# Optimization experiments

Hardware: AMD Instinct MI355X
Metric: run time of the kernel (lower is better)

## Reference

```python
import jax, jax.numpy as jnp
import numpy as np

B, S, D, H, HZ = 4096, 64, 9, 128, 32
DT = 0.1


def _lstm_cell(x, h, c, Wih, Whh, bih, bhh):
    gates = x @ Wih.T + bih + h @ Whh.T + bhh
    i, f, g, o = jnp.split(gates, 4, axis=-1)
    c_new = jax.nn.sigmoid(f) * c + jax.nn.sigmoid(i) * jnp.tanh(g)
    h_new = jax.nn.sigmoid(o) * jnp.tanh(c_new)
    return h_new, c_new


def _forward(input_batch, W_ih_enc, W_hh_enc, b_ih_enc, b_hh_enc, W_e, V_e, v_e,
             W_d, V_d, v_d, W_ih_dec, W_hh_dec, b_ih_dec, b_hh_dec,
             W_out, b_out, scaler_mean, scaler_std, pos_mean):
    bsz = input_batch.shape[0]
    # ---- encoder with input attention ----
    x_perm = jnp.swapaxes(input_batch, 1, 2)          # (B, D, S)
    attn_input = jnp.einsum('bds,ts->bdt', x_perm, V_e)  # V_e * x^i, precomputed once
    h0 = jnp.zeros((bsz, H), input_batch.dtype)
    c0 = jnp.zeros((bsz, H), input_batch.dtype)

    def enc_step(carry, x_t):
        h, c = carry
        attn_hidden = jnp.concatenate([h, c], axis=1) @ W_e.T          # (B, S)
        comb = jnp.tanh(attn_hidden[:, None, :] + attn_input)          # (B, D, S)
        e = comb @ v_e                                                 # (B, D)
        alpha = jax.nn.softmax(e, axis=1)
        h, c = _lstm_cell(alpha * x_t, h, c, W_ih_enc, W_hh_enc, b_ih_enc, b_hh_enc)
        return (h, c), h

    (h_enc, c_enc), hs = jax.lax.scan(enc_step, (h0, c0), jnp.swapaxes(input_batch, 0, 1))
    enc_hidden = jnp.swapaxes(hs, 0, 1)               # (B, S, H)
    attn_encoder = enc_hidden @ V_d.T                 # V_d * h_j, precomputed once

    # ---- initial physics state ----
    pos = input_batch[:, -1, :3] + pos_mean
    vel = input_batch[:, -1, 3:6] * scaler_std + scaler_mean
    pre_vel = input_batch[:, -2, 3:6] * scaler_std + scaler_mean
    acc = (vel - pre_vel) / DT

    def dec_step(carry, _):
        d, c, pos, vel, acc = carry
        attn_dec = jnp.concatenate([d, c], axis=1) @ W_d.T             # (B, H)
        comb = jnp.tanh(attn_dec[:, None, :] + attn_encoder)           # (B, S, H)
        beta = jax.nn.softmax(comb @ v_d, axis=1)                      # (B, S)
        context = jnp.einsum('bs,bsh->bh', beta, enc_hidden)           # (B, H)
        phys = jnp.concatenate([pos - pos_mean,
                                (vel - scaler_mean) / scaler_std,
                                acc / scaler_std], axis=1)             # (B, 9)
        d, c = _lstm_cell(jnp.concatenate([phys, context], axis=1), d, c,
                          W_ih_dec, W_hh_dec, b_ih_dec, b_hh_dec)
        pred_acc = (jnp.concatenate([d, context], axis=1) @ W_out.T + b_out) * scaler_std
        pos_pred = pos + vel * DT + 0.5 * acc * DT * DT                # Verlet position
        vel_new = vel + 0.5 * (acc + pred_acc) * DT                    # Verlet velocity
        out = jnp.concatenate([pos_pred, vel_new, pred_acc], axis=1)   # (B, 9)
        return (d, c, pos_pred, vel_new, pred_acc), out

    _, outs = jax.lax.scan(dec_step, (h_enc, c_enc, pos, vel, acc), None, length=HZ)
    return jnp.swapaxes(outs, 0, 1)                   # (B, HZ, 9)


def setup_inputs() -> dict:
    key = jax.random.key(0)
    ks = jax.random.split(key, 16)
    p = lambda k, shape, s=0.05: jax.random.normal(k, shape, dtype=jnp.float32) * s
    return dict(
        input_batch=jax.random.normal(ks[0], (B, S, D), dtype=jnp.float32),
        W_ih_enc=p(ks[1], (4 * H, D)), W_hh_enc=p(ks[2], (4 * H, H)),
        b_ih_enc=jnp.zeros((4 * H,), jnp.float32), b_hh_enc=jnp.zeros((4 * H,), jnp.float32),
        W_e=p(ks[3], (S, 2 * H)), V_e=p(ks[4], (S, S)), v_e=p(ks[5], (S,)),
        W_d=p(ks[6], (H, 2 * H)), V_d=p(ks[7], (H, H)), v_d=p(ks[8], (H,)),
        W_ih_dec=p(ks[9], (4 * H, 9 + H)), W_hh_dec=p(ks[10], (4 * H, H)),
        b_ih_dec=jnp.zeros((4 * H,), jnp.float32), b_hh_dec=jnp.zeros((4 * H,), jnp.float32),
        W_out=p(ks[11], (3, 2 * H)), b_out=jnp.zeros((3,), jnp.float32),
        scaler_mean=p(ks[12], (3,), 0.1),
        scaler_std=jnp.abs(p(ks[13], (3,), 0.1)) + 1.0,
        pos_mean=p(ks[14], (3,), 0.1),
    )


def reference(input_batch, W_ih_enc, W_hh_enc, b_ih_enc, b_hh_enc, W_e, V_e, v_e,
              W_d, V_d, v_d, W_ih_dec, W_hh_dec, b_ih_dec, b_hh_dec,
              W_out, b_out, scaler_mean, scaler_std, pos_mean):
    return _forward(input_batch, W_ih_enc, W_hh_enc, b_ih_enc, b_hh_enc, W_e, V_e, v_e,
                    W_d, V_d, v_d, W_ih_dec, W_hh_dec, b_ih_dec, b_hh_dec,
                    W_out, b_out, scaler_mean, scaler_std, pos_mean)
```

## Files before the change

### kernel.cpp

```cpp
#include <hip/hip_runtime.h>
#include <hip/hip_bf16.h>
#include <hip/hip_fp8.h>

#define B_   4096
#define S_   64
#define D_   9
#define H_   128
#define HZ_  32
#define DT_  0.1f

#define OFF_WET    0
#define OFF_VET    16384
#define OFF_WENCT  20480
#define OFF_BENC   90624
#define OFF_WDT    91136
#define OFF_WDECT  123904
#define OFF_BDEC   259584
#define OFF_WOUTT  260096
#define OFF_VDT    260864
#define OFF_DECD   277248
#define OFF_DECC   801536
#define F32_TOTAL  1325824
#define PREP_N     277248


typedef __bf16 bf16x8 __attribute__((ext_vector_type(8)));
typedef float  f32x4  __attribute__((ext_vector_type(4)));

__device__ __forceinline__ float fast_tanh(float x) {
    float e = __expf(2.0f * x);
    return 1.0f - __fdividef(2.0f, e + 1.0f);
}
__device__ __forceinline__ float sigf(float x) {
    return __fdividef(1.0f, 1.0f + __expf(-x));
}
__device__ __forceinline__ float bf_lo(unsigned int u) { return __uint_as_float(u << 16); }
__device__ __forceinline__ float bf_hi(unsigned int u) { return __uint_as_float(u & 0xffff0000u); }
__device__ __forceinline__ float bfu2f(unsigned short u) { return __uint_as_float((unsigned int)u << 16); }
__device__ __forceinline__ unsigned short f2bfu(float f) {
    __hip_bfloat16 b = __float2bfloat16(f);
    return *(unsigned short*)&b;
}
__device__ __forceinline__ unsigned int pack_bf(float lo, float hi) {
    return (unsigned int)f2bfu(lo) | ((unsigned int)f2bfu(hi) << 16);
}
__device__ __forceinline__ float f8tof(unsigned int byte) {
    __hip_fp8_e4m3 t; t.__x = (unsigned char)byte; return (float)t;
}
__device__ __forceinline__ unsigned char f2f8(float f) {
    __hip_fp8_e4m3 q(f); return q.__x;
}
__device__ __forceinline__ unsigned int pack4_f8(float a, float b, float c, float d) {
    return (unsigned int)f2f8(a) | ((unsigned int)f2f8(b) << 8) |
           ((unsigned int)f2f8(c) << 16) | ((unsigned int)f2f8(d) << 24);
}

__global__ void prep_kernel(const float* __restrict__ Wih_e, const float* __restrict__ Whh_e,
    const float* __restrict__ bih_e, const float* __restrict__ bhh_e,
    const float* __restrict__ W_e, const float* __restrict__ V_e,
    const float* __restrict__ W_d, const float* __restrict__ V_d,
    const float* __restrict__ Wih_d, const float* __restrict__ Whh_d,
    const float* __restrict__ bih_d, const float* __restrict__ bhh_d,
    const float* __restrict__ W_out, float* __restrict__ ws) {
  for (int idx = blockIdx.x * blockDim.x + threadIdx.x; idx < PREP_N;
       idx += gridDim.x * blockDim.x) {
    int i = idx;
    if (i < 16384) { continue; }
    i -= 16384;
    if (i < 4096) { int s = i >> 6, t = i & 63; ws[OFF_VET + i] = V_e[t * 64 + s]; continue; }
    i -= 4096;
    if (i < 70144) { continue; }
    i -= 70144;
    if (i < 512) { ws[OFF_BENC + i] = bih_e[i] + bhh_e[i]; continue; }
    i -= 512;
    if (i < 32768) { continue; }
    i -= 32768;
    if (i < 135680) { continue; }
    i -= 135680;
    if (i < 512) { ws[OFF_BDEC + i] = bih_d[i] + bhh_d[i]; continue; }
    i -= 512;
    if (i < 768) { int k = i / 3, j = i % 3; ws[OFF_WOUTT + i] = W_out[j * 256 + k]; continue; }
  }
}

__global__ void prep_mfma_kernel(const float* __restrict__ W_d,
    const float* __restrict__ Wih_d, const float* __restrict__ Whh_d,
    unsigned short* __restrict__ WdTm, unsigned short* __restrict__ WdecTm) {
  int idx = blockIdx.x * blockDim.x + threadIdx.x;
  if (idx < 32768) {
    int j = idx & 7, l = (idx >> 3) & 63, t = idx >> 9;
    int nt = t & 7, ks = t >> 3;
    int k = ks * 32 + (l >> 4) * 8 + j;
    int n = nt * 16 + (l & 15);
    WdTm[idx] = f2bfu(W_d[n * 256 + k]);
    return;
  }
  int i2 = idx - 32768;
  if (i2 < 147456) {
    int j = i2 & 7, l = (i2 >> 3) & 63, t = i2 >> 9;
    int ks = t % 9, tile = t / 9;
    int q = tile & 3, is = tile >> 2;
    int k = ks * 32 + (l >> 4) * 8 + j;
    int g = q * 128 + is * 16 + (l & 15);
    float v;
    if (k < 128)      v = Whh_d[g * 128 + k];
    else if (k < 256) v = Wih_d[g * 137 + 9 + (k - 128)];
    else if (k < 265) v = Wih_d[g * 137 + (k - 256)];
    else              v = 0.f;
    WdecTm[i2] = f2bfu(v);
  }
}

__global__ void prep_enc_mfma_kernel(const float* __restrict__ W_e,
    const float* __restrict__ Wih_e, const float* __restrict__ Whh_e,
    const float* __restrict__ V_d,
    unsigned short* __restrict__ WeTm, unsigned short* __restrict__ WencTm,
    unsigned short* __restrict__ VdTm) {
  int idx = blockIdx.x * blockDim.x + threadIdx.x;
  if (idx < 16384) {
    int j = idx & 7, l = (idx >> 3) & 63, tile = idx >> 9;
    int nt = tile & 3, ks = tile >> 2;
    int k = ks * 32 + (l >> 4) * 8 + j;
    int n = nt * 16 + (l & 15);
    WeTm[idx] = f2bfu(W_e[n * 256 + k]);
    return;
  }
  int i2 = idx - 16384;
  if (i2 < 81920) {
    int j = i2 & 7, l = (i2 >> 3) & 63, tile = i2 >> 9;
    int ks = tile % 5, tq = tile / 5;
    int q = tq & 3, is = tq >> 2;
    int kk = (l >> 4) * 8 + j;
    int g = q * 128 + is * 16 + (l & 15);
    float v;
    if (ks < 4) v = Whh_e[g * 128 + ks * 32 + kk];
    else        v = (kk < 9) ? Wih_e[g * 9 + kk] : 0.f;
    WencTm[i2] = f2bfu(v);
    return;
  }
  int i3 = i2 - 81920;
  if (i3 < 16384) {
    int j = i3 & 7, l = (i3 >> 3) & 63, tile = i3 >> 9;
    int nt = tile & 7, ks = tile >> 3;
    int i = ks * 32 + (l >> 4) * 8 + j;
    int n = nt * 16 + (l & 15);
    VdTm[i3] = f2bfu(V_d[n * 128 + i]);
  }
}

__global__ __launch_bounds__(512, 1) void encoder_mfma_kernel(
    const float* __restrict__ x_in, const float* __restrict__ ws,
    const float* __restrict__ v_e_g,
    const unsigned short* __restrict__ WeTm, const unsigned short* __restrict__ WencTm,
    __hip_bfloat16* __restrict__ EH,
    unsigned short* __restrict__ dG, float* __restrict__ cG) {
  __shared__ unsigned short hA[2][16 * 296];
  __shared__ float cF[16 * 132];
  __shared__ float ahL[16 * 64];
  __shared__ unsigned short aiL[16 * 576];
  __shared__ unsigned short xbL[16 * 576];

  const int tid = threadIdx.x;
  const int b0 = blockIdx.x * 16;
  const int l = tid & 63, w = tid >> 6;
  const int quad = l >> 4, l15 = l & 15;

  for (int i = tid; i < 16 * 576; i += 512) {
    int m = i / 576, r = i % 576;
    xbL[i] = f2bfu(x_in[(size_t)(b0 + m) * 576 + r]);
  }
  for (int i = tid; i < 2 * 16 * 296; i += 512) ((unsigned short*)hA)[i] = 0;
  for (int i = tid; i < 16 * 132; i += 512) cF[i] = 0.f;
  __syncthreads();

  {
    const float* __restrict__ VeT = ws + OFF_VET;
    for (int i = tid; i < 16 * 576; i += 512) {
      int t = i & 63, dd = (i >> 6) % 9, m = i / 576;
      float acc = 0.f;
      for (int s = 0; s < 64; ++s) acc += bfu2f(xbL[m * 576 + s * 9 + dd]) * VeT[s * 64 + t];
      aiL[m * 576 + dd * 64 + t] = f2bfu(acc);
    }
  }
  const float ve_r = v_e_g[l];
  const int ig = w * 16 + l15;
  float bbq[4];
  #pragma unroll
  for (int q = 0; q < 4; ++q) bbq[q] = ws[OFF_BENC + q * 128 + ig];
  __syncthreads();

  for (int t = 0; t < S_; ++t) {
    unsigned short* bufC = hA[t & 1];
    unsigned short* bufN = hA[(t + 1) & 1];
    if (w < 4) {
      f32x4 acc = {0.f, 0.f, 0.f, 0.f};
      #pragma unroll
      for (int ks = 0; ks < 8; ++ks) {
        uint4 au = *(const uint4*)&bufC[l15 * 296 + ks * 32 + quad * 8];
        uint4 bu = *(const uint4*)(WeTm + (size_t)((ks * 4 + w) * 64 + l) * 8);
        acc = __builtin_amdgcn_mfma_f32_16x16x32_bf16(
            __builtin_bit_cast(bf16x8, au), __builtin_bit_cast(bf16x8, bu), acc, 0, 0, 0);
      }
      #pragma unroll
      for (int r = 0; r < 4; ++r)
        ahL[(quad * 4 + r) * 64 + w * 16 + l15] = acc[r];
    }
    __syncthreads();
    {
      const int m0 = 2 * w, m1 = 2 * w + 1;
      float a0 = ahL[m0 * 64 + l], a1 = ahL[m1 * 64 + l];
      float e0k = -1e30f, e1k = -1e30f;
      #pragma unroll
      for (int dd = 0; dd < 9; ++dd) {
        float t0 = fast_tanh(a0 + bfu2f(aiL[m0 * 576 + dd * 64 + l])) * ve_r;
        float t1 = fast_tanh(a1 + bfu2f(aiL[m1 * 576 + dd * 64 + l])) * ve_r;
        #pragma unroll
        for (int off = 32; off; off >>= 1) {
          t0 += __shfl_xor(t0, off, 64);
          t1 += __shfl_xor(t1, off, 64);
        }
        if (l == dd) { e0k = t0; e1k = t1; }
      }
      float mx0 = e0k, mx1 = e1k;
      #pragma unroll
      for (int off = 8; off; off >>= 1) {
        mx0 = fmaxf(mx0, __shfl_xor(mx0, off, 64));
        mx1 = fmaxf(mx1, __shfl_xor(mx1, off, 64));
      }
      float ex0 = (l < 9) ? __expf(e0k - mx0) : 0.f;
      float ex1 = (l < 9) ? __expf(e1k - mx1) : 0.f;
      float s0 = ex0, s1 = ex1;
      #pragma unroll
      for (int off = 8; off; off >>= 1) {
        s0 += __shfl_xor(s0, off, 64);
        s1 += __shfl_xor(s1, off, 64);
      }
      if (l < 9) {
        bufC[m0 * 296 + 256 + l] = f2bfu(__fdividef(ex0, s0) * bfu2f(xbL[m0 * 576 + t * 9 + l]));
        bufC[m1 * 296 + 256 + l] = f2bfu(__fdividef(ex1, s1) * bfu2f(xbL[m1 * 576 + t * 9 + l]));
      }
    }
    __syncthreads();
    {
      uint4 af[5];
      #pragma unroll
      for (int ks = 0; ks < 4; ++ks)
        af[ks] = *(const uint4*)&bufC[l15 * 296 + ks * 32 + quad * 8];
      af[4] = *(const uint4*)&bufC[l15 * 296 + 256 + quad * 8];
      f32x4 g4[4];
      #pragma unroll
      for (int q = 0; q < 4; ++q) {
        f32x4 acc = {0.f, 0.f, 0.f, 0.f};
        #pragma unroll
        for (int ks = 0; ks < 5; ++ks) {
          uint4 bu = *(const uint4*)(WencTm + (size_t)(((w * 4 + q) * 5 + ks) * 64 + l) * 8);
          acc = __builtin_amdgcn_mfma_f32_16x16x32_bf16(
              __builtin_bit_cast(bf16x8, af[ks]), __builtin_bit_cast(bf16x8, bu), acc, 0, 0, 0);
        }
        g4[q] = acc;
      }
      #pragma unroll
      for (int r = 0; r < 4; ++r) {
        int m = quad * 4 + r;
        float gi = g4[0][r] + bbq[0];
        float gf = g4[1][r] + bbq[1];
        float gg = g4[2][r] + bbq[2];
        float go = g4[3][r] + bbq[3];
        float co = cF[m * 132 + ig];
        float cn = sigf(gf) * co + sigf(gi) * fast_tanh(gg);
        float hn = sigf(go) * fast_tanh(cn);
        cF[m * 132 + ig] = cn;
        bufN[m * 296 + ig] = f2bfu(hn);
        bufN[m * 296 + 128 + ig] = f2bfu(cn);
        EH[((size_t)(b0 + m) * S_ + t) * H_ + ig] = __float2bfloat16(hn);
      }
    }
    __syncthreads();
  }
  for (int i = tid; i < 16 * 128; i += 512) {
    int m = i >> 7, ii = i & 127;
    dG[(size_t)(b0 + m) * 128 + ii] = hA[0][m * 296 + ii];
    cG[(size_t)(b0 + m) * 128 + ii] = cF[m * 132 + ii];
  }
}

__global__ __launch_bounds__(256) void attnenc_mfma_kernel(
    const unsigned short* __restrict__ EH, const unsigned short* __restrict__ VdTm,
    unsigned char* __restrict__ AETf8, unsigned char* __restrict__ EHf8) {
  const int tid = threadIdx.x;
  const int b = blockIdx.x * 4 + (tid >> 6);
  const int l = tid & 63;
  const int quad = l >> 4, l15 = l & 15;

  const unsigned short* ehb = EH + (size_t)b * 8192;
  uint4 A[4][4];
  #pragma unroll
  for (int st = 0; st < 4; ++st)
    #pragma unroll
    for (int ks = 0; ks < 4; ++ks)
      A[st][ks] = *(const uint4*)(ehb + (st * 16 + l15) * 128 + ks * 32 + quad * 8);

  {
    unsigned char* e8b = EHf8 + (size_t)b * 8192;
    #pragma unroll
    for (int st = 0; st < 4; ++st)
      #pragma unroll
      for (int ks = 0; ks < 4; ++ks) {
        uint4 a = A[st][ks];
        uint2 pk;
        pk.x = pack4_f8(bf_lo(a.x), bf_hi(a.x), bf_lo(a.y), bf_hi(a.y));
        pk.y = pack4_f8(bf_lo(a.z), bf_hi(a.z), bf_lo(a.w), bf_hi(a.w));
        *(uint2*)(e8b + (st * 16 + l15) * 128 + ks * 32 + quad * 8) = pk;
      }
  }

  unsigned char* outb = AETf8 + (size_t)b * 8192;
  const int k = l15;
  #pragma unroll
  for (int nt = 0; nt < 8; ++nt) {
    uint4 Bf[4];
    #pragma unroll
    for (int ks = 0; ks < 4; ++ks)
      Bf[ks] = *(const uint4*)(VdTm + (size_t)((ks * 8 + nt) * 64 + l) * 8);
    int kg = nt * 16 + k;
    int kb = kg >> 3, k7 = kg & 7;
    #pragma unroll
    for (int st = 0; st < 4; ++st) {
      f32x4 acc = {0.f, 0.f, 0.f, 0.f};
      #pragma unroll
      for (int ks = 0; ks < 4; ++ks)
        acc = __builtin_amdgcn_mfma_f32_16x16x32_bf16(
            __builtin_bit_cast(bf16x8, A[st][ks]), __builtin_bit_cast(bf16x8, Bf[ks]), acc, 0, 0, 0);
      #pragma unroll
      for (int r = 0; r < 4; ++r) {
        int s = st * 16 + quad * 4 + r;
        outb[kb * 512 + s * 8 + k7] = f2f8(acc[r]);
      }
    }
  }
}

__global__ __launch_bounds__(256) void init_dec_kernel(
    const float* __restrict__ x_in,
    const unsigned short* __restrict__ dG, const float* __restrict__ cG,
    const unsigned short* __restrict__ WdTm,
    const float* __restrict__ smean_g, const float* __restrict__ sstd_g,
    const float* __restrict__ pmean_g,
    unsigned short* __restrict__ adG, float* __restrict__ pvsG) {
  __shared__ unsigned short dcB[16 * 264];
  const int tid = threadIdx.x;
  const int b0 = blockIdx.x * 16;
  const int l = tid & 63, w = tid >> 6;
  const int quad = l >> 4, l15 = l & 15;

  {
    int m = tid >> 4, i0 = (tid & 15) * 8;
    *(uint4*)&dcB[m * 264 + i0] = *(const uint4*)(dG + (size_t)(b0 + m) * 128 + i0);
    float4 c0 = *(const float4*)(cG + (size_t)(b0 + m) * 128 + i0);
    float4 c1 = *(const float4*)(cG + (size_t)(b0 + m) * 128 + i0 + 4);
    uint4 pk;
    pk.x = pack_bf(c0.x, c0.y); pk.y = pack_bf(c0.z, c0.w);
    pk.z = pack_bf(c1.x, c1.y); pk.w = pack_bf(c1.z, c1.w);
    *(uint4*)&dcB[m * 264 + 128 + i0] = pk;
  }
  if (tid < 48) {
    int m = tid / 3, jj = tid % 3;
    const float* xi = x_in + (size_t)(b0 + m) * 576;
    float sm = smean_g[jj], ss = sstd_g[jj], pm = pmean_g[jj];
    float v  = xi[63 * 9 + 3 + jj] * ss + sm;
    float pv = xi[62 * 9 + 3 + jj] * ss + sm;
    float* P = pvsG + (size_t)(b0 + m) * 12;
    P[jj] = xi[63 * 9 + jj] + pm;
    P[3 + jj] = v;
    P[6 + jj] = (v - pv) / DT_;
  }
  __syncthreads();
  #pragma unroll
  for (int t = 0; t < 2; ++t) {
    const int nt = w + 4 * t;
    f32x4 acc = {0.f, 0.f, 0.f, 0.f};
    #pragma unroll
    for (int ks = 0; ks < 8; ++ks) {
      uint4 au = *(const uint4*)&dcB[l15 * 264 + ks * 32 + quad * 8];
      uint4 bu = *(const uint4*)(WdTm + (size_t)((ks * 8 + nt) * 64 + l) * 8);
      acc = __builtin_amdgcn_mfma_f32_16x16x32_bf16(
          __builtin_bit_cast(bf16x8, au), __builtin_bit_cast(bf16x8, bu), acc, 0, 0, 0);
    }
    int n = nt * 16 + l15;
    #pragma unroll
    for (int r = 0; r < 4; ++r)
      adG[(size_t)(b0 + quad * 4 + r) * 128 + n] = f2bfu(acc[r]);
  }
}

__global__ __launch_bounds__(256, 8) void attn_step_kernel(
    const unsigned char* __restrict__ AETf8, const unsigned char* __restrict__ EHf8,
    const unsigned short* __restrict__ adG, const float* __restrict__ v_d_g,
    unsigned short* __restrict__ ctxG) {
  __shared__ unsigned short adL[2 * 128];
  __shared__ float vdL[128];
  __shared__ float scp[2][2][64];
  __shared__ float bet[2][64];
  __shared__ float ctxP[2][2][128];

  const int tid = threadIdx.x;
  const int b0 = blockIdx.x * 2;
  const int l = tid & 63, w = tid >> 6;
  const int ml = w >> 1, half = w & 1;
  const int quad = l >> 4, l15 = l & 15;

  if (tid < 32)
    *(uint4*)&adL[tid * 8] = *(const uint4*)(adG + (size_t)(b0 + (tid >> 4)) * 128 + (tid & 15) * 8);
  if (tid < 128) vdL[tid] = v_d_g[tid];
  __syncthreads();

  {
    const unsigned char* aet = AETf8 + (size_t)(b0 + ml) * 8192 + (size_t)half * 8 * 512;
    const unsigned short* adp = adL + ml * 128 + half * 64;
    float e = 0.f;
    #pragma unroll
    for (int kb = 0; kb < 8; ++kb) {
      uint2 av = *(const uint2*)(aet + kb * 512 + l * 8);
      uint4 ad8 = *(const uint4*)(adp + kb * 8);
      float4 v0 = *(const float4*)&vdL[half * 64 + kb * 8];
      float4 v1 = *(const float4*)&vdL[half * 64 + kb * 8 + 4];
      e += fast_tanh(bf_lo(ad8.x) + f8tof(av.x))       * v0.x;
      e += fast_tanh(bf_hi(ad8.x) + f8tof(av.x >> 8))  * v0.y;
      e += fast_tanh(bf_lo(ad8.y) + f8tof(av.x >> 16)) * v0.z;
      e += fast_tanh(bf_hi(ad8.y) + f8tof(av.x >> 24)) * v0.w;
      e += fast_tanh(bf_lo(ad8.z) + f8tof(av.y))       * v1.x;
      e += fast_tanh(bf_hi(ad8.z) + f8tof(av.y >> 8))  * v1.y;
      e += fast_tanh(bf_lo(ad8.w) + f8tof(av.y >> 16)) * v1.z;
      e += fast_tanh(bf_hi(ad8.w) + f8tof(av.y >> 24)) * v1.w;
    }
    scp[ml][half][l] = e;
  }
  __syncthreads();
  if (half == 0) {
    float e = scp[ml][0][l] + scp[ml][1][l];
    float mx = e;
    #pragma unroll
    for (int off = 32; off; off >>= 1) mx = fmaxf(mx, __shfl_xor(mx, off, 64));
    float ex = __expf(e - mx);
    float ss = ex;
    #pragma unroll
    for (int off = 32; off; off >>= 1) ss += __shfl_xor(ss, off, 64);
    bet[ml][l] = __fdividef(ex, ss);
  }
  __syncthreads();
  {
    const unsigned char* base = EHf8 + (size_t)(b0 + ml) * 8192 + (size_t)half * 32 * 128;
    float a[8];
    #pragma unroll
    for (int r = 0; r < 8; ++r) a[r] = 0.f;
    #pragma unroll
    for (int it = 0; it < 8; ++it) {
      int sl = it * 4 + quad;
      uint2 ev = *(const uint2*)(base + sl * 128 + l15 * 8);
      float bt = bet[ml][half * 32 + sl];
      a[0] += bt * f8tof(ev.x);       a[1] += bt * f8tof(ev.x >> 8);
      a[2] += bt * f8tof(ev.x >> 16); a[3] += bt * f8tof(ev.x >> 24);
      a[4] += bt * f8tof(ev.y);       a[5] += bt * f8tof(ev.y >> 8);
      a[6] += bt * f8tof(ev.y >> 16); a[7] += bt * f8tof(ev.y >> 24);
    }
    #pragma unroll
    for (int r = 0; r < 8; ++r) {
      a[r] += __shfl_xor(a[r], 16, 64);
      a[r] += __shfl_xor(a[r], 32, 64);
    }
    if (quad == 0) {
      *(float4*)&ctxP[ml][half][l15 * 8]     = make_float4(a[0], a[1], a[2], a[3]);
      *(float4*)&ctxP[ml][half][l15 * 8 + 4] = make_float4(a[4], a[5], a[6], a[7]);
    }
  }
  __syncthreads();
  if (tid < 128) {
    int mi = tid >> 6, hp = (tid & 63) * 2;
    float c0 = ctxP[mi][0][hp]     + ctxP[mi][1][hp];
    float c1 = ctxP[mi][0][hp + 1] + ctxP[mi][1][hp + 1];
    *(unsigned int*)(ctxG + (size_t)(b0 + mi) * 128 + hp) = pack_bf(c0, c1);
  }
}

__global__ __launch_bounds__(512, 2) void gemm_step_kernel(
    const float* __restrict__ ws,
    const unsigned short* __restrict__ dG_in, float* __restrict__ cG,
    const unsigned short* __restrict__ ctxG,
    const unsigned short* __restrict__ WdTm, const unsigned short* __restrict__ WdecTm,
    unsigned short* __restrict__ dG_out, unsigned short* __restrict__ adG,
    float* __restrict__ pvsG,
    const float* __restrict__ b_out_g, const float* __restrict__ smean_g,
    const float* __restrict__ sstd_g, const float* __restrict__ pmean_g,
    float* __restrict__ out, int hz) {
  __shared__ unsigned short gA[16 * 296];
  __shared__ unsigned short dcB[16 * 264];
  __shared__ float pd[16 * 3 * 8];
  __shared__ float pc[16 * 3 * 4];

  const int tid = threadIdx.x;
  const int b0 = blockIdx.x * 16;
  const int l = tid & 63, w = tid >> 6;
  const int quad = l >> 4, l15 = l & 15;

  if (tid < 256) {
    int m = tid >> 4, i0 = (tid & 15) * 8;
    *(uint4*)&gA[m * 296 + i0] = *(const uint4*)(dG_in + (size_t)(b0 + m) * 128 + i0);
  } else {
    int t = tid - 256;
    int m = t >> 4, i0 = (t & 15) * 8;
    *(uint4*)&gA[m * 296 + 128 + i0] = *(const uint4*)(ctxG + (size_t)(b0 + m) * 128 + i0);
  }
  if (tid < 496) { int mm = tid / 31, r = tid % 31; gA[mm * 296 + 265 + r] = 0; }
  if (tid < 48) {
    int m = tid / 3, jj = tid % 3;
    const float* P = pvsG + (size_t)(b0 + m) * 12;
    float sm = smean_g[jj], ss = sstd_g[jj], pm = pmean_g[jj];
    gA[m * 296 + 256 + jj]     = f2bfu(P[jj] - pm);
    gA[m * 296 + 256 + 3 + jj] = f2bfu((P[3 + jj] - sm) / ss);
    gA[m * 296 + 256 + 6 + jj] = f2bfu(P[6 + jj] / ss);
  }
  __syncthreads();

  {
    uint4 af[9];
    #pragma unroll
    for (int ks = 0; ks < 9; ++ks)
      af[ks] = *(const uint4*)&gA[l15 * 296 + ks * 32 + quad * 8];
    const int is = w, i = is * 16 + l15;
    float bb[4], wd[3];
    #pragma unroll
    for (int q = 0; q < 4; ++q) bb[q] = ws[OFF_BDEC + q * 128 + i];
    #pragma unroll
    for (int jj = 0; jj < 3; ++jj) wd[jj] = ws[OFF_WOUTT + i * 3 + jj];
    f32x4 g4[4];
    #pragma unroll
    for (int q = 0; q < 4; ++q) {
      f32x4 acc = {0.f, 0.f, 0.f, 0.f};
      #pragma unroll
      for (int ks = 0; ks < 9; ++ks) {
        uint4 bu = *(const uint4*)(WdecTm + (size_t)(((is * 4 + q) * 9 + ks) * 64 + l) * 8);
        acc = __builtin_amdgcn_mfma_f32_16x16x32_bf16(
            __builtin_bit_cast(bf16x8, af[ks]), __builtin_bit_cast(bf16x8, bu), acc, 0, 0, 0);
      }
      g4[q] = acc;
    }
    float pr[4][3];
    #pragma unroll
    for (int r = 0; r < 4; ++r) {
      int m = quad * 4 + r;
      float gi = g4[0][r] + bb[0];
      float gf = g4[1][r] + bb[1];
      float gg = g4[2][r] + bb[2];
      float go = g4[3][r] + bb[3];
      float co = cG[(size_t)(b0 + m) * 128 + i];
      float cn = sigf(gf) * co + sigf(gi) * fast_tanh(gg);
      float hn = sigf(go) * fast_tanh(cn);
      cG[(size_t)(b0 + m) * 128 + i] = cn;
      unsigned short hb = f2bfu(hn);
      dG_out[(size_t)(b0 + m) * 128 + i] = hb;
      dcB[m * 264 + i] = hb;
      dcB[m * 264 + 128 + i] = f2bfu(cn);
      pr[r][0] = hn * wd[0]; pr[r][1] = hn * wd[1]; pr[r][2] = hn * wd[2];
    }
    #pragma unroll
    for (int r = 0; r < 4; ++r)
      #pragma unroll
      for (int jj = 0; jj < 3; ++jj) {
        float v = pr[r][jj];
        #pragma unroll
        for (int off = 8; off; off >>= 1) v += __shfl_xor(v, off, 64);
        pr[r][jj] = v;
      }
    if (l15 == 0) {
      #pragma unroll
      for (int r = 0; r < 4; ++r)
        #pragma unroll
        for (int jj = 0; jj < 3; ++jj)
          pd[((quad * 4 + r) * 3 + jj) * 8 + is] = pr[r][jj];
    }
  }
  __syncthreads();

  {
    const int nt = w;
    f32x4 acc = {0.f, 0.f, 0.f, 0.f};
    #pragma unroll
    for (int ks = 0; ks < 8; ++ks) {
      uint4 au = *(const uint4*)&dcB[l15 * 264 + ks * 32 + quad * 8];
      uint4 bu = *(const uint4*)(WdTm + (size_t)((ks * 8 + nt) * 64 + l) * 8);
      acc = __builtin_amdgcn_mfma_f32_16x16x32_bf16(
          __builtin_bit_cast(bf16x8, au), __builtin_bit_cast(bf16x8, bu), acc, 0, 0, 0);
    }
    int n = nt * 16 + l15;
    #pragma unroll
    for (int r = 0; r < 4; ++r) {
      int m = quad * 4 + r;
      adG[(size_t)(b0 + m) * 128 + n] = f2bfu(acc[r]);
    }
  }
  if (tid < 192) {
    int m = tid / 12, jj = (tid % 12) / 4, part = tid % 4;
    int k0 = part * 32;
    float acc = 0.f;
    for (int k = k0; k < k0 + 32; ++k) {
      __hip_bfloat16 hv = *(__hip_bfloat16*)&gA[m * 296 + 128 + k];
      acc += __bfloat162float(hv) * ws[OFF_WOUTT + 384 + k * 3 + jj];
    }
    pc[(m * 3 + jj) * 4 + part] = acc;
  }
  __syncthreads();

  if (tid < 48) {
    int m = tid / 3, jj = tid % 3;
    float s = b_out_g[jj];
    #pragma unroll
    for (int p = 0; p < 4; ++p) s += pc[(m * 3 + jj) * 4 + p];
    #pragma unroll
    for (int is = 0; is < 8; ++is) s += pd[(m * 3 + jj) * 8 + is];
    float pacc = s * sstd_g[jj];
    float* P = pvsG + (size_t)(b0 + m) * 12;
    float pos = P[jj], vel = P[3 + jj], acc = P[6 + jj];
    float ppred = pos + vel * DT_ + 0.5f * acc * DT_ * DT_;
    float vnew  = vel + 0.5f * (acc + pacc) * DT_;
    size_t ob = ((size_t)(b0 + m) * HZ_ + hz) * 9;
    out[ob + jj] = ppred; out[ob + 3 + jj] = vnew; out[ob + 6 + jj] = pacc;
    P[jj] = ppred; P[3 + jj] = vnew; P[6 + jj] = pacc;
  }
}

extern "C" void kernel_launch(void* const* d_in, const int* in_sizes, int n_in,
                              void* d_out, int out_size, void* d_ws, size_t ws_size,
                              hipStream_t stream) {
  (void)in_sizes; (void)n_in; (void)out_size; (void)ws_size;
  const float* x      = (const float*)d_in[0];
  const float* Wih_e  = (const float*)d_in[1];
  const float* Whh_e  = (const float*)d_in[2];
  const float* bih_e  = (const float*)d_in[3];
  const float* bhh_e  = (const float*)d_in[4];
  const float* W_e    = (const float*)d_in[5];
  const float* V_e    = (const float*)d_in[6];
  const float* v_e    = (const float*)d_in[7];
  const float* W_d    = (const float*)d_in[8];
  const float* V_d    = (const float*)d_in[9];
  const float* v_d    = (const float*)d_in[10];
  const float* Wih_d  = (const float*)d_in[11];
  const float* Whh_d  = (const float*)d_in[12];
  const float* bih_d  = (const float*)d_in[13];
  const float* bhh_d  = (const float*)d_in[14];
  const float* W_out  = (const float*)d_in[15];
  const float* b_out  = (const float*)d_in[16];
  const float* smean  = (const float*)d_in[17];
  const float* sstd   = (const float*)d_in[18];
  const float* pmean  = (const float*)d_in[19];

  float* ws = (float*)d_ws;
  float* pvsG = ws;
  unsigned short* WeTm   = (unsigned short*)(ws + OFF_WET);
  unsigned short* WencTm = (unsigned short*)(ws + OFF_WENCT);
  unsigned short* WdTm   = (unsigned short*)(ws + OFF_WDT);
  unsigned short* WdecTm = (unsigned short*)(ws + OFF_WDECT);
  unsigned short* VdTm   = (unsigned short*)(ws + OFF_VDT);
  unsigned short* dG     = (unsigned short*)(ws + OFF_DECD);
  unsigned short* ctxG   = dG + 524288;
  float* cG = ws + OFF_DECC;
  unsigned short* ub  = (unsigned short*)(ws + F32_TOTAL);
  unsigned short* EH  = ub;
  unsigned char*  AETf8 = (unsigned char*)(ub + 33554432);
  unsigned char*  EHf8  = AETf8 + (size_t)B_ * 8192;
  unsigned short* adG = ub + 67108864;
  float* out = (float*)d_out;

  prep_kernel<<<(PREP_N + 255) / 256, 256, 0, stream>>>(
      Wih_e, Whh_e, bih_e, bhh_e, W_e, V_e, W_d, V_d,
      Wih_d, Whh_d, bih_d, bhh_d, W_out, ws);
  prep_mfma_kernel<<<(32768 + 147456 + 255) / 256, 256, 0, stream>>>(
      W_d, Wih_d, Whh_d, WdTm, WdecTm);
  prep_enc_mfma_kernel<<<(16384 + 81920 + 16384 + 255) / 256, 256, 0, stream>>>(
      W_e, Wih_e, Whh_e, V_d, WeTm, WencTm, VdTm);
  encoder_mfma_kernel<<<B_ / 16, 512, 0, stream>>>(
      x, ws, v_e, WeTm, WencTm, (__hip_bfloat16*)EH, dG, cG);
  attnenc_mfma_kernel<<<B_ / 4, 256, 0, stream>>>(EH, VdTm, AETf8, EHf8);
  init_dec_kernel<<<B_ / 16, 256, 0, stream>>>(
      x, dG, cG, WdTm, smean, sstd, pmean, adG, pvsG);
  for (int hz = 0; hz < HZ_; ++hz) {
    attn_step_kernel<<<B_ / 2, 256, 0, stream>>>(AETf8, EHf8, adG, v_d, ctxG);
    gemm_step_kernel<<<B_ / 16, 512, 0, stream>>>(
        ws, dG, cG, ctxG, WdTm, WdecTm, dG, adG, pvsG,
        b_out, smean, sstd, pmean, out, hz);
  }
}
```

Measured before the change: 1.687 ms.

## Fuse decoder init and all horizon steps into one persistent kernel

Replaces the per-step attention and GEMM kernel launches (64 launches plus init) with a single kernel in which each block owns 4 batch rows and loops over all 32 horizon steps. The attention-encoder tile and the decoder hidden, cell and physics state stay in shared memory instead of round-tripping through global memory between launches. The cost is MFMA tiles that are only a quarter full (4 of 16 rows used), so weight loads per row rise, and the large shared-memory footprint limits occupancy to few blocks per CU.

```diff
diff --git a/kernel.cpp b/kernel.cpp
--- a/kernel.cpp
+++ b/kernel.cpp
@@ -22,7 +22,6 @@
 #define OFF_DECC   801536
 #define F32_TOTAL  1325824
 #define PREP_N     277248
-
 
 typedef __bf16 bf16x8 __attribute__((ext_vector_type(8)));
 typedef float  f32x4  __attribute__((ext_vector_type(4)));
@@ -340,44 +339,86 @@
   }
 }
 
-__global__ __launch_bounds__(256) void init_dec_kernel(
-    const float* __restrict__ x_in,
+__global__ __launch_bounds__(256, 2) void dec_fused_kernel(
+    const float* __restrict__ ws,
+    const unsigned char* __restrict__ AETf8, const unsigned char* __restrict__ EHf8,
     const unsigned short* __restrict__ dG, const float* __restrict__ cG,
-    const unsigned short* __restrict__ WdTm,
+    const unsigned short* __restrict__ WdTm, const unsigned short* __restrict__ WdecTm,
+    const float* __restrict__ v_d_g, const float* __restrict__ b_out_g,
     const float* __restrict__ smean_g, const float* __restrict__ sstd_g,
     const float* __restrict__ pmean_g,
-    unsigned short* __restrict__ adG, float* __restrict__ pvsG) {
+    const float* __restrict__ x_in,
+    float* __restrict__ out) {
+  __shared__ unsigned char  AET[4][8192];
+  __shared__ unsigned short gA[16 * 296];
   __shared__ unsigned short dcB[16 * 264];
+  __shared__ float          cL[4 * 128];
+  __shared__ unsigned short adL[4 * 128];
+  __shared__ float          bet[4][64];
+  __shared__ float          vdL[128];
+  __shared__ float          pcs[4 * 3 * 8];
+  __shared__ float          pvs[4 * 12];
+
   const int tid = threadIdx.x;
-  const int b0 = blockIdx.x * 16;
+  const int b0 = blockIdx.x * 4;
   const int l = tid & 63, w = tid >> 6;
   const int quad = l >> 4, l15 = l & 15;
 
+  for (int i = tid; i < 16 * 296; i += 256) gA[i] = 0;
+  for (int i = tid; i < 16 * 264; i += 256) dcB[i] = 0;
   {
+    const uint4* src = (const uint4*)(AETf8 + (size_t)b0 * 8192);
+    uint4* dst = (uint4*)AET;
+    for (int i = tid; i < 2048; i += 256) dst[i] = src[i];
+  }
+  if (tid < 128) vdL[tid] = v_d_g[tid];
+  __syncthreads();
+
+  if (tid < 64) {
     int m = tid >> 4, i0 = (tid & 15) * 8;
-    *(uint4*)&dcB[m * 264 + i0] = *(const uint4*)(dG + (size_t)(b0 + m) * 128 + i0);
+    uint4 dv = *(const uint4*)(dG + (size_t)(b0 + m) * 128 + i0);
+    *(uint4*)&gA[m * 296 + i0] = dv;
+    *(uint4*)&dcB[m * 264 + i0] = dv;
     float4 c0 = *(const float4*)(cG + (size_t)(b0 + m) * 128 + i0);
     float4 c1 = *(const float4*)(cG + (size_t)(b0 + m) * 128 + i0 + 4);
+    *(float4*)&cL[m * 128 + i0] = c0;
+    *(float4*)&cL[m * 128 + i0 + 4] = c1;
     uint4 pk;
     pk.x = pack_bf(c0.x, c0.y); pk.y = pack_bf(c0.z, c0.w);
     pk.z = pack_bf(c1.x, c1.y); pk.w = pack_bf(c1.z, c1.w);
     *(uint4*)&dcB[m * 264 + 128 + i0] = pk;
   }
-  if (tid < 48) {
+  if (tid < 12) {
     int m = tid / 3, jj = tid % 3;
     const float* xi = x_in + (size_t)(b0 + m) * 576;
     float sm = smean_g[jj], ss = sstd_g[jj], pm = pmean_g[jj];
     float v  = xi[63 * 9 + 3 + jj] * ss + sm;
     float pv = xi[62 * 9 + 3 + jj] * ss + sm;
-    float* P = pvsG + (size_t)(b0 + m) * 12;
-    P[jj] = xi[63 * 9 + jj] + pm;
-    P[3 + jj] = v;
-    P[6 + jj] = (v - pv) / DT_;
+    float pos = xi[63 * 9 + jj] + pm;
+    float ac = (v - pv) / DT_;
+    float* P = pvs + m * 12;
+    P[jj] = pos; P[3 + jj] = v; P[6 + jj] = ac;
+    gA[m * 296 + 256 + jj]     = f2bfu(pos - pm);
+    gA[m * 296 + 256 + 3 + jj] = f2bfu((v - sm) / ss);
+    gA[m * 296 + 256 + 6 + jj] = f2bfu(ac / ss);
+  }
+  float bb[2][4];
+  #pragma unroll
+  for (int t2 = 0; t2 < 2; ++t2) {
+    int i = (w + 4 * t2) * 16 + l15;
+    #pragma unroll
+    for (int q = 0; q < 4; ++q) bb[t2][q] = ws[OFF_BDEC + q * 128 + i];
+  }
+  float k_sm = 0.f, k_ss = 1.f, k_pm = 0.f, k_bo = 0.f;
+  if (tid < 12) {
+    int jj = tid % 3;
+    k_sm = smean_g[jj]; k_ss = sstd_g[jj]; k_pm = pmean_g[jj]; k_bo = b_out_g[jj];
   }
   __syncthreads();
+
   #pragma unroll
-  for (int t = 0; t < 2; ++t) {
-    const int nt = w + 4 * t;
+  for (int t2 = 0; t2 < 2; ++t2) {
+    const int nt = w + 4 * t2;
     f32x4 acc = {0.f, 0.f, 0.f, 0.f};
     #pragma unroll
     for (int ks = 0; ks < 8; ++ks) {
@@ -386,245 +427,161 @@
       acc = __builtin_amdgcn_mfma_f32_16x16x32_bf16(
           __builtin_bit_cast(bf16x8, au), __builtin_bit_cast(bf16x8, bu), acc, 0, 0, 0);
     }
-    int n = nt * 16 + l15;
-    #pragma unroll
-    for (int r = 0; r < 4; ++r)
-      adG[(size_t)(b0 + quad * 4 + r) * 128 + n] = f2bfu(acc[r]);
-  }
-}
-
-__global__ __launch_bounds__(256, 8) void attn_step_kernel(
-    const unsigned char* __restrict__ AETf8, const unsigned char* __restrict__ EHf8,
-    const unsigned short* __restrict__ adG, const float* __restrict__ v_d_g,
-    unsigned short* __restrict__ ctxG) {
-  __shared__ unsigned short adL[2 * 128];
-  __shared__ float vdL[128];
-  __shared__ float scp[2][2][64];
-  __shared__ float bet[2][64];
-  __shared__ float ctxP[2][2][128];
-
-  const int tid = threadIdx.x;
-  const int b0 = blockIdx.x * 2;
-  const int l = tid & 63, w = tid >> 6;
-  const int ml = w >> 1, half = w & 1;
-  const int quad = l >> 4, l15 = l & 15;
-
-  if (tid < 32)
-    *(uint4*)&adL[tid * 8] = *(const uint4*)(adG + (size_t)(b0 + (tid >> 4)) * 128 + (tid & 15) * 8);
-  if (tid < 128) vdL[tid] = v_d_g[tid];
+    if (quad == 0) {
+      int n = nt * 16 + l15;
+      #pragma unroll
+      for (int r = 0; r < 4; ++r) adL[r * 128 + n] = f2bfu(acc[r]);
+    }
+  }
   __syncthreads();
 
-  {
-    const unsigned char* aet = AETf8 + (size_t)(b0 + ml) * 8192 + (size_t)half * 8 * 512;
-    const unsigned short* adp = adL + ml * 128 + half * 64;
-    float e = 0.f;
-    #pragma unroll
-    for (int kb = 0; kb < 8; ++kb) {
-      uint2 av = *(const uint2*)(aet + kb * 512 + l * 8);
-      uint4 ad8 = *(const uint4*)(adp + kb * 8);
-      float4 v0 = *(const float4*)&vdL[half * 64 + kb * 8];
-      float4 v1 = *(const float4*)&vdL[half * 64 + kb * 8 + 4];
-      e += fast_tanh(bf_lo(ad8.x) + f8tof(av.x))       * v0.x;
-      e += fast_tanh(bf_hi(ad8.x) + f8tof(av.x >> 8))  * v0.y;
-      e += fast_tanh(bf_lo(ad8.y) + f8tof(av.x >> 16)) * v0.z;
-      e += fast_tanh(bf_hi(ad8.y) + f8tof(av.x >> 24)) * v0.w;
-      e += fast_tanh(bf_lo(ad8.z) + f8tof(av.y))       * v1.x;
-      e += fast_tanh(bf_hi(ad8.z) + f8tof(av.y >> 8))  * v1.y;
-      e += fast_tanh(bf_lo(ad8.w) + f8tof(av.y >> 16)) * v1.z;
-      e += fast_tanh(bf_hi(ad8.w) + f8tof(av.y >> 24)) * v1.w;
-    }
-    scp[ml][half][l] = e;
-  }
-  __syncthreads();
-  if (half == 0) {
-    float e = scp[ml][0][l] + scp[ml][1][l];
-    float mx = e;
-    #pragma unroll
-    for (int off = 32; off; off >>= 1) mx = fmaxf(mx, __shfl_xor(mx, off, 64));
-    float ex = __expf(e - mx);
-    float ss = ex;
-    #pragma unroll
-    for (int off = 32; off; off >>= 1) ss += __shfl_xor(ss, off, 64);
-    bet[ml][l] = __fdividef(ex, ss);
-  }
-  __syncthreads();
-  {
-    const unsigned char* base = EHf8 + (size_t)(b0 + ml) * 8192 + (size_t)half * 32 * 128;
-    float a[8];
-    #pragma unroll
-    for (int r = 0; r < 8; ++r) a[r] = 0.f;
-    #pragma unroll
-    for (int it = 0; it < 8; ++it) {
-      int sl = it * 4 + quad;
-      uint2 ev = *(const uint2*)(base + sl * 128 + l15 * 8);
-      float bt = bet[ml][half * 32 + sl];
-      a[0] += bt * f8tof(ev.x);       a[1] += bt * f8tof(ev.x >> 8);
-      a[2] += bt * f8tof(ev.x >> 16); a[3] += bt * f8tof(ev.x >> 24);
-      a[4] += bt * f8tof(ev.y);       a[5] += bt * f8tof(ev.y >> 8);
-      a[6] += bt * f8tof(ev.y >> 16); a[7] += bt * f8tof(ev.y >> 24);
-    }
-    #pragma unroll
-    for (int r = 0; r < 8; ++r) {
-      a[r] += __shfl_xor(a[r], 16, 64);
-      a[r] += __shfl_xor(a[r], 32, 64);
-    }
-    if (quad == 0) {
-      *(float4*)&ctxP[ml][half][l15 * 8]     = make_float4(a[0], a[1], a[2], a[3]);
-      *(float4*)&ctxP[ml][half][l15 * 8 + 4] = make_float4(a[4], a[5], a[6], a[7]);
-    }
-  }
-  __syncthreads();
-  if (tid < 128) {
-    int mi = tid >> 6, hp = (tid & 63) * 2;
-    float c0 = ctxP[mi][0][hp]     + ctxP[mi][1][hp];
-    float c1 = ctxP[mi][0][hp + 1] + ctxP[mi][1][hp + 1];
-    *(unsigned int*)(ctxG + (size_t)(b0 + mi) * 128 + hp) = pack_bf(c0, c1);
-  }
-}
-
-__global__ __launch_bounds__(512, 2) void gemm_step_kernel(
-    const float* __restrict__ ws,
-    const unsigned short* __restrict__ dG_in, float* __restrict__ cG,
-    const unsigned short* __restrict__ ctxG,
-    const unsigned short* __restrict__ WdTm, const unsigned short* __restrict__ WdecTm,
-    unsigned short* __restrict__ dG_out, unsigned short* __restrict__ adG,
-    float* __restrict__ pvsG,
-    const float* __restrict__ b_out_g, const float* __restrict__ smean_g,
-    const float* __restrict__ sstd_g, const float* __restrict__ pmean_g,
-    float* __restrict__ out, int hz) {
-  __shared__ unsigned short gA[16 * 296];
-  __shared__ unsigned short dcB[16 * 264];
-  __shared__ float pd[16 * 3 * 8];
-  __shared__ float pc[16 * 3 * 4];
-
-  const int tid = threadIdx.x;
-  const int b0 = blockIdx.x * 16;
-  const int l = tid & 63, w = tid >> 6;
-  const int quad = l >> 4, l15 = l & 15;
-
-  if (tid < 256) {
-    int m = tid >> 4, i0 = (tid & 15) * 8;
-    *(uint4*)&gA[m * 296 + i0] = *(const uint4*)(dG_in + (size_t)(b0 + m) * 128 + i0);
-  } else {
-    int t = tid - 256;
-    int m = t >> 4, i0 = (t & 15) * 8;
-    *(uint4*)&gA[m * 296 + 128 + i0] = *(const uint4*)(ctxG + (size_t)(b0 + m) * 128 + i0);
-  }
-  if (tid < 496) { int mm = tid / 31, r = tid % 31; gA[mm * 296 + 265 + r] = 0; }
-  if (tid < 48) {
-    int m = tid / 3, jj = tid % 3;
-    const float* P = pvsG + (size_t)(b0 + m) * 12;
-    float sm = smean_g[jj], ss = sstd_g[jj], pm = pmean_g[jj];
-    gA[m * 296 + 256 + jj]     = f2bfu(P[jj] - pm);
-    gA[m * 296 + 256 + 3 + jj] = f2bfu((P[3 + jj] - sm) / ss);
-    gA[m * 296 + 256 + 6 + jj] = f2bfu(P[6 + jj] / ss);
-  }
-  __syncthreads();
-
-  {
+  for (int hz = 0; hz < HZ_; ++hz) {
+    {
+      const unsigned char* aet = AET[w];
+      float e = 0.f;
+      #pragma unroll
+      for (int kb = 0; kb < 16; ++kb) {
+        uint2 av = *(const uint2*)(aet + kb * 512 + l * 8);
+        uint4 ad8 = *(const uint4*)(adL + w * 128 + kb * 8);
+        float4 v0 = *(const float4*)&vdL[kb * 8];
+        float4 v1 = *(const float4*)&vdL[kb * 8 + 4];
+        e += fast_tanh(bf_lo(ad8.x) + f8tof(av.x))       * v0.x;
+        e += fast_tanh(bf_hi(ad8.x) + f8tof(av.x >> 8))  * v0.y;
+        e += fast_tanh(bf_lo(ad8.y) + f8tof(av.x >> 16)) * v0.z;
+        e += fast_tanh(bf_hi(ad8.y) + f8tof(av.x >> 24)) * v0.w;
+        e += fast_tanh(bf_lo(ad8.z) + f8tof(av.y))       * v1.x;
+        e += fast_tanh(bf_hi(ad8.z) + f8tof(av.y >> 8))  * v1.y;
+        e += fast_tanh(bf_lo(ad8.w) + f8tof(av.y >> 16)) * v1.z;
+        e += fast_tanh(bf_hi(ad8.w) + f8tof(av.y >> 24)) * v1.w;
+      }
+      float mx = e;
+      #pragma unroll
+      for (int off = 32; off; off >>= 1) mx = fmaxf(mx, __shfl_xor(mx, off, 64));
+      float ex = __expf(e - mx);
+      float sm = ex;
+      #pragma unroll
+      for (int off = 32; off; off >>= 1) sm += __shfl_xor(sm, off, 64);
+      bet[w][l] = __fdividef(ex, sm);
+    }
+    __syncthreads();
+
+    {
+      const unsigned char* ehb = EHf8 + (size_t)(b0 + w) * 8192;
+      const int i0 = l15 * 8;
+      float a[8];
+      #pragma unroll
+      for (int r = 0; r < 8; ++r) a[r] = 0.f;
+      #pragma unroll
+      for (int it = 0; it < 16; ++it) {
+        int s = quad * 16 + it;
+        uint2 ev = *(const uint2*)(ehb + s * 128 + i0);
+        float bt = bet[w][s];
+        a[0] += bt * f8tof(ev.x);       a[1] += bt * f8tof(ev.x >> 8);
+        a[2] += bt * f8tof(ev.x >> 16); a[3] += bt * f8tof(ev.x >> 24);
+        a[4] += bt * f8tof(ev.y);       a[5] += bt * f8tof(ev.y >> 8);
+        a[6] += bt * f8tof(ev.y >> 16); a[7] += bt * f8tof(ev.y >> 24);
+      }
+      #pragma unroll
+      for (int r = 0; r < 8; ++r) {
+        a[r] += __shfl_xor(a[r], 16, 64);
+        a[r] += __shfl_xor(a[r], 32, 64);
+      }
+      if (quad == 0) {
+        uint4 pk;
+        pk.x = pack_bf(a[0], a[1]); pk.y = pack_bf(a[2], a[3]);
+        pk.z = pack_bf(a[4], a[5]); pk.w = pack_bf(a[6], a[7]);
+        *(uint4*)&gA[w * 296 + 128 + i0] = pk;
+      }
+    }
+    __syncthreads();
+
     uint4 af[9];
     #pragma unroll
     for (int ks = 0; ks < 9; ++ks)
       af[ks] = *(const uint4*)&gA[l15 * 296 + ks * 32 + quad * 8];
-    const int is = w, i = is * 16 + l15;
-    float bb[4], wd[3];
-    #pragma unroll
-    for (int q = 0; q < 4; ++q) bb[q] = ws[OFF_BDEC + q * 128 + i];
-    #pragma unroll
-    for (int jj = 0; jj < 3; ++jj) wd[jj] = ws[OFF_WOUTT + i * 3 + jj];
-    f32x4 g4[4];
-    #pragma unroll
-    for (int q = 0; q < 4; ++q) {
+    __syncthreads();
+
+    #pragma unroll
+    for (int t2 = 0; t2 < 2; ++t2) {
+      const int is = w + 4 * t2;
+      const int i = is * 16 + l15;
+      f32x4 g4[4];
+      #pragma unroll
+      for (int q = 0; q < 4; ++q) {
+        f32x4 acc = {0.f, 0.f, 0.f, 0.f};
+        #pragma unroll
+        for (int ks = 0; ks < 9; ++ks) {
+          uint4 bu = *(const uint4*)(WdecTm + (size_t)(((is * 4 + q) * 9 + ks) * 64 + l) * 8);
+          acc = __builtin_amdgcn_mfma_f32_16x16x32_bf16(
+              __builtin_bit_cast(bf16x8, af[ks]), __builtin_bit_cast(bf16x8, bu), acc, 0, 0, 0);
+        }
+        g4[q] = acc;
+      }
+      if (quad == 0) {
+        #pragma unroll
+        for (int r = 0; r < 4; ++r) {
+          float gi = g4[0][r] + bb[t2][0];
+          float gf = g4[1][r] + bb[t2][1];
+          float gg = g4[2][r] + bb[t2][2];
+          float go = g4[3][r] + bb[t2][3];
+          float co = cL[r * 128 + i];
+          float cn = sigf(gf) * co + sigf(gi) * fast_tanh(gg);
+          float hn = sigf(go) * fast_tanh(cn);
+          cL[r * 128 + i] = cn;
+          unsigned short hb = f2bfu(hn);
+          gA[r * 296 + i] = hb;
+          dcB[r * 264 + i] = hb;
+          dcB[r * 264 + 128 + i] = f2bfu(cn);
+        }
+      }
+    }
+    __syncthreads();
+
+    #pragma unroll
+    for (int t2 = 0; t2 < 2; ++t2) {
+      const int nt = w + 4 * t2;
       f32x4 acc = {0.f, 0.f, 0.f, 0.f};
       #pragma unroll
-      for (int ks = 0; ks < 9; ++ks) {
-        uint4 bu = *(const uint4*)(WdecTm + (size_t)(((is * 4 + q) * 9 + ks) * 64 + l) * 8);
+      for (int ks = 0; ks < 8; ++ks) {
+        uint4 au = *(const uint4*)&dcB[l15 * 264 + ks * 32 + quad * 8];
+        uint4 bu = *(const uint4*)(WdTm + (size_t)((ks * 8 + nt) * 64 + l) * 8);
         acc = __builtin_amdgcn_mfma_f32_16x16x32_bf16(
-            __builtin_bit_cast(bf16x8, af[ks]), __builtin_bit_cast(bf16x8, bu), acc, 0, 0, 0);
-      }
-      g4[q] = acc;
-    }
-    float pr[4][3];
-    #pragma unroll
-    for (int r = 0; r < 4; ++r) {
-      int m = quad * 4 + r;
-      float gi = g4[0][r] + bb[0];
-      float gf = g4[1][r] + bb[1];
-      float gg = g4[2][r] + bb[2];
-      float go = g4[3][r] + bb[3];
-      float co = cG[(size_t)(b0 + m) * 128 + i];
-      float cn = sigf(gf) * co + sigf(gi) * fast_tanh(gg);
-      float hn = sigf(go) * fast_tanh(cn);
-      cG[(size_t)(b0 + m) * 128 + i] = cn;
-      unsigned short hb = f2bfu(hn);
-      dG_out[(size_t)(b0 + m) * 128 + i] = hb;
-      dcB[m * 264 + i] = hb;
-      dcB[m * 264 + 128 + i] = f2bfu(cn);
-      pr[r][0] = hn * wd[0]; pr[r][1] = hn * wd[1]; pr[r][2] = hn * wd[2];
-    }
-    #pragma unroll
-    for (int r = 0; r < 4; ++r)
-      #pragma unroll
-      for (int jj = 0; jj < 3; ++jj) {
-        float v = pr[r][jj];
+            __builtin_bit_cast(bf16x8, au), __builtin_bit_cast(bf16x8, bu), acc, 0, 0, 0);
+      }
+      if (quad == 0) {
+        int n = nt * 16 + l15;
         #pragma unroll
-        for (int off = 8; off; off >>= 1) v += __shfl_xor(v, off, 64);
-        pr[r][jj] = v;
-      }
-    if (l15 == 0) {
-      #pragma unroll
-      for (int r = 0; r < 4; ++r)
-        #pragma unroll
-        for (int jj = 0; jj < 3; ++jj)
-          pd[((quad * 4 + r) * 3 + jj) * 8 + is] = pr[r][jj];
-    }
-  }
-  __syncthreads();
-
-  {
-    const int nt = w;
-    f32x4 acc = {0.f, 0.f, 0.f, 0.f};
-    #pragma unroll
-    for (int ks = 0; ks < 8; ++ks) {
-      uint4 au = *(const uint4*)&dcB[l15 * 264 + ks * 32 + quad * 8];
-      uint4 bu = *(const uint4*)(WdTm + (size_t)((ks * 8 + nt) * 64 + l) * 8);
-      acc = __builtin_amdgcn_mfma_f32_16x16x32_bf16(
-          __builtin_bit_cast(bf16x8, au), __builtin_bit_cast(bf16x8, bu), acc, 0, 0, 0);
-    }
-    int n = nt * 16 + l15;
-    #pragma unroll
-    for (int r = 0; r < 4; ++r) {
-      int m = quad * 4 + r;
-      adG[(size_t)(b0 + m) * 128 + n] = f2bfu(acc[r]);
-    }
-  }
-  if (tid < 192) {
-    int m = tid / 12, jj = (tid % 12) / 4, part = tid % 4;
-    int k0 = part * 32;
-    float acc = 0.f;
-    for (int k = k0; k < k0 + 32; ++k) {
-      __hip_bfloat16 hv = *(__hip_bfloat16*)&gA[m * 296 + 128 + k];
-      acc += __bfloat162float(hv) * ws[OFF_WOUTT + 384 + k * 3 + jj];
-    }
-    pc[(m * 3 + jj) * 4 + part] = acc;
-  }
-  __syncthreads();
-
-  if (tid < 48) {
-    int m = tid / 3, jj = tid % 3;
-    float s = b_out_g[jj];
-    #pragma unroll
-    for (int p = 0; p < 4; ++p) s += pc[(m * 3 + jj) * 4 + p];
-    #pragma unroll
-    for (int is = 0; is < 8; ++is) s += pd[(m * 3 + jj) * 8 + is];
-    float pacc = s * sstd_g[jj];
-    float* P = pvsG + (size_t)(b0 + m) * 12;
-    float pos = P[jj], vel = P[3 + jj], acc = P[6 + jj];
-    float ppred = pos + vel * DT_ + 0.5f * acc * DT_ * DT_;
-    float vnew  = vel + 0.5f * (acc + pacc) * DT_;
-    size_t ob = ((size_t)(b0 + m) * HZ_ + hz) * 9;
-    out[ob + jj] = ppred; out[ob + 3 + jj] = vnew; out[ob + 6 + jj] = pacc;
-    P[jj] = ppred; P[3 + jj] = vnew; P[6 + jj] = pacc;
+        for (int r = 0; r < 4; ++r) adL[r * 128 + n] = f2bfu(acc[r]);
+      }
+    }
+    if (tid < 96) {
+      int m = tid / 24, r2 = tid % 24, jj = r2 >> 3, part = r2 & 7;
+      float acc = 0.f;
+      #pragma unroll 4
+      for (int k = part * 32; k < part * 32 + 32; ++k)
+        acc += bfu2f(gA[m * 296 + k]) * ws[OFF_WOUTT + k * 3 + jj];
+      pcs[(m * 3 + jj) * 8 + part] = acc;
+    }
+    __syncthreads();
+
+    if (tid < 12) {
+      int m = tid / 3, jj = tid % 3;
+      float s = k_bo;
+      #pragma unroll
+      for (int p = 0; p < 8; ++p) s += pcs[(m * 3 + jj) * 8 + p];
+      float pacc = s * k_ss;
+      float* P = pvs + m * 12;
+      float pos = P[jj], vel = P[3 + jj], ac = P[6 + jj];
+      float ppred = pos + vel * DT_ + 0.5f * ac * DT_ * DT_;
+      float vnew  = vel + 0.5f * (ac + pacc) * DT_;
+      size_t ob = ((size_t)(b0 + m) * HZ_ + hz) * 9;
+      out[ob + jj] = ppred; out[ob + 3 + jj] = vnew; out[ob + 6 + jj] = pacc;
+      P[jj] = ppred; P[3 + jj] = vnew; P[6 + jj] = pacc;
+      gA[m * 296 + 256 + jj]     = f2bfu(ppred - k_pm);
+      gA[m * 296 + 256 + 3 + jj] = f2bfu((vnew - k_sm) / k_ss);
+      gA[m * 296 + 256 + 6 + jj] = f2bfu(pacc / k_ss);
+    }
+    __syncthreads();
   }
 }
 
@@ -654,20 +611,17 @@
   const float* pmean  = (const float*)d_in[19];
 
   float* ws = (float*)d_ws;
-  float* pvsG = ws;
   unsigned short* WeTm   = (unsigned short*)(ws + OFF_WET);
   unsigned short* WencTm = (unsigned short*)(ws + OFF_WENCT);
   unsigned short* WdTm   = (unsigned short*)(ws + OFF_WDT);
   unsigned short* WdecTm = (unsigned short*)(ws + OFF_WDECT);
   unsigned short* VdTm   = (unsigned short*)(ws + OFF_VDT);
   unsigned short* dG     = (unsigned short*)(ws + OFF_DECD);
-  unsigned short* ctxG   = dG + 524288;
   float* cG = ws + OFF_DECC;
   unsigned short* ub  = (unsigned short*)(ws + F32_TOTAL);
   unsigned short* EH  = ub;
   unsigned char*  AETf8 = (unsigned char*)(ub + 33554432);
   unsigned char*  EHf8  = AETf8 + (size_t)B_ * 8192;
-  unsigned short* adG = ub + 67108864;
   float* out = (float*)d_out;
 
   prep_kernel<<<(PREP_N + 255) / 256, 256, 0, stream>>>(
@@ -680,12 +634,7 @@
   encoder_mfma_kernel<<<B_ / 16, 512, 0, stream>>>(
       x, ws, v_e, WeTm, WencTm, (__hip_bfloat16*)EH, dG, cG);
   attnenc_mfma_kernel<<<B_ / 4, 256, 0, stream>>>(EH, VdTm, AETf8, EHf8);
-  init_dec_kernel<<<B_ / 16, 256, 0, stream>>>(
-      x, dG, cG, WdTm, smean, sstd, pmean, adG, pvsG);
-  for (int hz = 0; hz < HZ_; ++hz) {
-    attn_step_kernel<<<B_ / 2, 256, 0, stream>>>(AETf8, EHf8, adG, v_d, ctxG);
-    gemm_step_kernel<<<B_ / 16, 512, 0, stream>>>(
-        ws, dG, cG, ctxG, WdTm, WdecTm, dG, adG, pvsG,
-        b_out, smean, sstd, pmean, out, hz);
-  }
-}
+  dec_fused_kernel<<<B_ / 4, 256, 0, stream>>>(
+      ws, AETf8, EHf8, dG, cG, WdTm, WdecTm,
+      v_d, b_out, smean, sstd, pmean, x, out);
+}
```

Measured after the change: 3.330 ms. 97.3% more time.
